# Optimization experiments

Hardware: AMD Instinct MI355X
Metric: run time of the kernel (lower is better)

## Reference

```python
import jax, jax.numpy as jnp
import numpy as np

W = 4  # kernel_size

def setup_inputs() -> dict:
    key = jax.random.key(0)
    k1, k2, k3, k4 = jax.random.split(key, 4)
    B, T, D, H = 4, 4096, 2048, 256
    x = jax.random.normal(k1, (B, T, D), dtype=jnp.float32)
    # stored as [in, out] (transpose of torch Linear convention)
    w1 = jax.random.normal(k2, (D, H), dtype=jnp.float32) * 0.02
    w2 = jax.random.normal(k3, (H, D * W), dtype=jnp.float32) * 0.02
    b2 = jax.random.normal(k4, (D * W,), dtype=jnp.float32) * 0.02
    return {"x": x, "w1": w1, "w2": w2, "b2": b2}

def reference(x, w1, w2, b2):
    # x: [B, T, D]
    B, T, D = x.shape
    # kernel generator: Linear -> silu -> Linear(+bias)
    h = jax.nn.silu(jnp.einsum('btd,dh->bth', x, w1))
    flat = jnp.einsum('bth,ho->bto', h, w2) + b2          # [B, T, D*W]
    kernels = flat.reshape(B, T, D, W)                    # per-token depthwise kernels
    # causal depthwise dynamic conv: out[t] = sum_w k[t, :, w] * x[t - (W-1) + w]
    xp = jnp.pad(x, ((0, 0), (W - 1, 0), (0, 0)))         # left-pad time by W-1
    out = jnp.zeros_like(x)
    for w in range(W):  # W is a small static constant (4)
        out = out + kernels[..., w] * xp[:, w:w + T, :]
    return jax.nn.silu(out)
```

## Files before the change

### kernel.cpp

```cpp
#include <hip/hip_runtime.h>

typedef unsigned short u16;
typedef unsigned int   u32;
typedef __attribute__((ext_vector_type(8))) short short8;
typedef __attribute__((ext_vector_type(4))) float floatx4;

#define T_DIM 4096
#define D_DIM 2048
#define H_DIM 256
#define M_DIM 16384
#define NFLAT 8192

__device__ __forceinline__ u16 f2bf(float f) {
  union { float f; u32 u; } c; c.f = f;
  u32 x = c.u;
  x += 0x7FFFu + ((x >> 16) & 1u);
  return (u16)(x >> 16);
}
__device__ __forceinline__ u32 pk2(float a, float b) {
  return (u32)f2bf(a) | ((u32)f2bf(b) << 16);
}

__device__ __forceinline__ void glds16(const void* g, void* l) {
  __builtin_amdgcn_global_load_lds(
      (const __attribute__((address_space(1))) void*)g,
      (__attribute__((address_space(3))) void*)l, 16, 0, 0);
}

__global__ void __launch_bounds__(256) tr_cvt_all(const float* __restrict__ w1,
                                                  u16* __restrict__ w1t,
                                                  const float* __restrict__ w2,
                                                  u16* __restrict__ w2t) {
  __shared__ u16 tile[32][33];
  int bid = blockIdx.x;
  const float* src; u16* dst; int R, C, c0, r0;
  if (bid < 512) {
    src = w1; dst = w1t; R = D_DIM; C = H_DIM;
    c0 = (bid & 7) * 32; r0 = (bid >> 3) * 32;
  } else {
    int b = bid - 512;
    src = w2; dst = w2t; R = H_DIM; C = NFLAT;
    c0 = (b & 255) * 32; r0 = (b >> 8) * 32;
  }
  const int tx = threadIdx.x & 31;
  const int ty = threadIdx.x >> 5;
  #pragma unroll
  for (int i = ty; i < 32; i += 8)
    tile[i][tx] = f2bf(src[(size_t)(r0 + i) * C + (c0 + tx)]);
  __syncthreads();
  #pragma unroll
  for (int i = ty; i < 32; i += 8)
    dst[(size_t)(c0 + i) * R + (r0 + tx)] = tile[tx][i];
}

__global__ void __launch_bounds__(256) gemm1_silu(const float* __restrict__ X,
                                                  const u16* __restrict__ Bt,
                                                  u16* __restrict__ H) {
  __shared__ __align__(16) u16 As[2][64][64];
  __shared__ __align__(16) u16 Bs[2][64][64];
  const int tid  = threadIdx.x;
  const int lane = tid & 63, l15 = lane & 15, quad = lane >> 4;
  const int wv   = tid >> 6, wy = wv >> 1, wx = wv & 1;
  const int lin  = blockIdx.x + blockIdx.y * 4;
  const int wgid = (lin & 7) * 128 + (lin >> 3);
  const int m0   = (wgid >> 2) * 64;
  const int n0   = (wgid & 3) * 64;
  const int srow = lane >> 3, sc = lane & 7;

  floatx4 acc[2][2];
  const floatx4 zf = {0.f, 0.f, 0.f, 0.f};
  #pragma unroll
  for (int i = 0; i < 2; ++i)
    #pragma unroll
    for (int j = 0; j < 2; ++j) acc[i][j] = zf;

  float4 fA[2][2];

#define G1_LOADA(KT)                                                          \
  _Pragma("unroll")                                                           \
  for (int i = 0; i < 2; ++i) {                                               \
    int s = i * 256 + tid, row = s >> 3, g = s & 7;                           \
    const float* xs = &X[(size_t)(m0 + row) * D_DIM + (KT) * 64 + g * 8];     \
    fA[i][0] = *(const float4*)xs;                                            \
    fA[i][1] = *(const float4*)(xs + 4);                                      \
  }

#define G1_WRITEA(BUF)                                                        \
  _Pragma("unroll")                                                           \
  for (int i = 0; i < 2; ++i) {                                               \
    int s = i * 256 + tid, row = s >> 3, g = s & 7, c = g ^ (row & 7);        \
    uint4 pk;                                                                 \
    pk.x = pk2(fA[i][0].x, fA[i][0].y);                                       \
    pk.y = pk2(fA[i][0].z, fA[i][0].w);                                       \
    pk.z = pk2(fA[i][1].x, fA[i][1].y);                                       \
    pk.w = pk2(fA[i][1].z, fA[i][1].w);                                       \
    *(uint4*)&As[BUF][row][c * 8] = pk;                                       \
  }

#define G1_STAGEB(KT, BUF)                                                    \
  _Pragma("unroll")                                                           \
  for (int ci = 0; ci < 2; ++ci) {                  \
    int ch  = wv * 2 + ci;                                                    \
    int row = ch * 8 + srow;                                                  \
    glds16(&Bt[(size_t)(n0 + row) * D_DIM + (KT) * 64 + (sc ^ (row & 7)) * 8],\
           (char*)Bs + (BUF) * 8192 + ch * 1024);                             \
  }

  G1_LOADA(0);
  G1_STAGEB(0, 0);
  G1_WRITEA(0);
  G1_LOADA(1);
  __syncthreads();

  #pragma unroll 2
  for (int t = 0; t < 32; ++t) {
    const int b = t & 1;
    if (t + 1 < 32) {
      G1_WRITEA(b ^ 1);
      G1_STAGEB(t + 1, b ^ 1);
    }
    if (t + 2 < 32) G1_LOADA(t + 2);
    short8 af[2][2], bfr[2][2];
    #pragma unroll
    for (int ks = 0; ks < 2; ++ks) {
      #pragma unroll
      for (int mi = 0; mi < 2; ++mi) {
        int row = wy * 32 + mi * 16 + l15;
        af[mi][ks] = *(const short8*)&As[b][row][((ks * 4 + quad) ^ (row & 7)) * 8];
      }
      #pragma unroll
      for (int ni = 0; ni < 2; ++ni) {
        int row = wx * 32 + ni * 16 + l15;
        bfr[ni][ks] = *(const short8*)&Bs[b][row][((ks * 4 + quad) ^ (row & 7)) * 8];
      }
    }
    #pragma unroll
    for (int ks = 0; ks < 2; ++ks)
      #pragma unroll
      for (int mi = 0; mi < 2; ++mi)
        #pragma unroll
        for (int ni = 0; ni < 2; ++ni)
          acc[mi][ni] = __builtin_amdgcn_mfma_f32_16x16x32_bf16(af[mi][ks], bfr[ni][ks], acc[mi][ni], 0, 0, 0);
    if (t + 1 < 32) __syncthreads();
  }

  #pragma unroll
  for (int mi = 0; mi < 2; ++mi)
    #pragma unroll
    for (int ni = 0; ni < 2; ++ni)
      #pragma unroll
      for (int r = 0; r < 4; ++r) {
        float v = acc[mi][ni][r];
        v = v / (1.f + __expf(-v));
        int row = m0 + wy * 32 + mi * 16 + quad * 4 + r;
        int col = n0 + wx * 32 + ni * 16 + l15;
        H[(size_t)row * H_DIM + col] = f2bf(v);
      }
#undef G1_LOADA
#undef G1_WRITEA
#undef G1_STAGEB
}

__global__ void __launch_bounds__(256) gemm2_conv_silu(const u16* __restrict__ Hin,
                                                       const u16* __restrict__ Bt,
                                                       const float* __restrict__ bias,
                                                       const float* __restrict__ X,
                                                       float* __restrict__ Out) {
  __shared__ __align__(16) u16 As[128][64];
  __shared__ __align__(16) u16 Bs[128][64];
  const int tid  = threadIdx.x;
  const int lane = tid & 63, l15 = lane & 15, quad = lane >> 4;
  const int wv   = tid >> 6, wy = wv >> 1, wx = wv & 1;
  const int lin  = blockIdx.x + blockIdx.y * 64;
  const int wgid = (lin & 7) * 1024 + (lin >> 3);
  const int m0   = (wgid >> 6) * 128;
  const int d0   = (wgid & 63) * 32;
  const int srow = lane >> 3, sc = lane & 7;

  floatx4 acc[4][4];
  const floatx4 zf = {0.f, 0.f, 0.f, 0.f};
  #pragma unroll
  for (int i = 0; i < 4; ++i)
    #pragma unroll
    for (int j = 0; j < 4; ++j) acc[i][j] = zf;

  for (int k0 = 0; k0 < H_DIM; k0 += 64) {
    __syncthreads();
    #pragma unroll
    for (int ci = 0; ci < 4; ++ci) {
      int ch  = ci * 4 + wv;
      int row = ch * 8 + srow;
      int g   = (sc ^ (row & 7)) * 8;
      glds16(&Hin[(size_t)(m0 + row) * H_DIM + k0 + g], (char*)As + ch * 1024);
      int fc = (d0 + ((row >> 6) << 4) + (row & 15)) * 4 + ((row >> 4) & 3);
      glds16(&Bt[(size_t)fc * H_DIM + k0 + g], (char*)Bs + ch * 1024);
    }
    __syncthreads();
    short8 af[4][2], bfr[4][2];
    #pragma unroll
    for (int ks = 0; ks < 2; ++ks) {
      #pragma unroll
      for (int mi = 0; mi < 4; ++mi) {
        int row = wy * 64 + mi * 16 + l15;
        af[mi][ks] = *(const short8*)&As[row][((ks * 4 + quad) ^ (row & 7)) * 8];
      }
      #pragma unroll
      for (int ni = 0; ni < 4; ++ni) {
        int row = wx * 64 + ni * 16 + l15;
        bfr[ni][ks] = *(const short8*)&Bs[row][((ks * 4 + quad) ^ (row & 7)) * 8];
      }
    }
    #pragma unroll
    for (int ks = 0; ks < 2; ++ks)
      #pragma unroll
      for (int mi = 0; mi < 4; ++mi)
        #pragma unroll
        for (int ni = 0; ni < 4; ++ni)
          acc[mi][ni] = __builtin_amdgcn_mfma_f32_16x16x32_bf16(af[mi][ks], bfr[ni][ks], acc[mi][ni], 0, 0, 0);
  }

  const int d     = d0 + wx * 16 + l15;
  const float4 bv = *(const float4*)&bias[(size_t)d * 4];
  const int tbase = m0 & (T_DIM - 1);
  const int bbase = m0 - tbase;
  const float* xcol = &X[(size_t)bbase * D_DIM + d];
  float* ocol       = &Out[(size_t)m0 * D_DIM + d];

  #pragma unroll
  for (int mi = 0; mi < 4; ++mi) {
    int t0 = wy * 64 + mi * 16 + quad * 4;
    int tq = tbase + t0;
    float xv[7];
    #pragma unroll
    for (int j = 0; j < 7; ++j) {
      int tt = tq - 3 + j;
      xv[j] = (tt >= 0) ? xcol[(size_t)tt * D_DIM] : 0.f;
    }
    #pragma unroll
    for (int r = 0; r < 4; ++r) {
      float c0 = acc[mi][0][r] + bv.x;
      float c1 = acc[mi][1][r] + bv.y;
      float c2 = acc[mi][2][r] + bv.z;
      float c3 = acc[mi][3][r] + bv.w;
      float o  = c0 * xv[r] + c1 * xv[r + 1] + c2 * xv[r + 2] + c3 * xv[r + 3];
      float y  = o / (1.f + __expf(-o));
      ocol[(size_t)(t0 + r) * D_DIM] = y;
    }
  }
}

extern "C" void kernel_launch(void* const* d_in, const int* in_sizes, int n_in,
                              void* d_out, int out_size, void* d_ws, size_t ws_size,
                              hipStream_t stream) {
  const float* x  = (const float*)d_in[0];
  const float* w1 = (const float*)d_in[1];
  const float* w2 = (const float*)d_in[2];
  const float* b2 = (const float*)d_in[3];
  float* out = (float*)d_out;

  u16* w1t = (u16*)d_ws;
  u16* w2t = w1t + (size_t)H_DIM * D_DIM;
  u16* h   = w2t + (size_t)NFLAT * H_DIM;

  tr_cvt_all<<<512 + 2048, 256, 0, stream>>>(w1, w1t, w2, w2t);
  gemm1_silu<<<dim3(4, M_DIM / 64), 256, 0, stream>>>(x, w1t, h);
  gemm2_conv_silu<<<dim3(D_DIM / 32, M_DIM / 128), 256, 0, stream>>>(h, w2t, b2, x, out);
}
```

Before: 380.8 us.

## Retile gemm1 to full-H 32-row tiles so X is read once

gemm1 now assigns each block 32 rows of X and all 256 H columns, with each wave owning 64 output columns. Before, four blocks per 64-row strip each re-read the same fp32 X rows, so X traffic drops roughly fourfold. The cost is a larger B tile staged in LDS per k-step (64KB double-buffered) and more accumulators per wave, which may lower occupancy. The XCD-aware block swizzles in both GEMMs are also removed in favour of plain block indexing.

```diff
diff --git a/kernel.cpp b/kernel.cpp
--- a/kernel.cpp
+++ b/kernel.cpp
@@ -56,54 +56,49 @@
 __global__ void __launch_bounds__(256) gemm1_silu(const float* __restrict__ X,
                                                   const u16* __restrict__ Bt,
                                                   u16* __restrict__ H) {
-  __shared__ __align__(16) u16 As[2][64][64];
-  __shared__ __align__(16) u16 Bs[2][64][64];
+  __shared__ __align__(16) u16 As[2][32][64];
+  __shared__ __align__(16) u16 Bs[2][256][64];
   const int tid  = threadIdx.x;
   const int lane = tid & 63, l15 = lane & 15, quad = lane >> 4;
-  const int wv   = tid >> 6, wy = wv >> 1, wx = wv & 1;
-  const int lin  = blockIdx.x + blockIdx.y * 4;
-  const int wgid = (lin & 7) * 128 + (lin >> 3);
-  const int m0   = (wgid >> 2) * 64;
-  const int n0   = (wgid & 3) * 64;
+  const int wv   = tid >> 6;
+  const int m0   = blockIdx.x * 32;
   const int srow = lane >> 3, sc = lane & 7;
 
-  floatx4 acc[2][2];
+  floatx4 acc[2][4];
   const floatx4 zf = {0.f, 0.f, 0.f, 0.f};
   #pragma unroll
   for (int i = 0; i < 2; ++i)
     #pragma unroll
-    for (int j = 0; j < 2; ++j) acc[i][j] = zf;
-
-  float4 fA[2][2];
+    for (int j = 0; j < 4; ++j) acc[i][j] = zf;
+
+  float4 fA[2];
 
 #define G1_LOADA(KT)                                                          \
-  _Pragma("unroll")                                                           \
-  for (int i = 0; i < 2; ++i) {                                               \
-    int s = i * 256 + tid, row = s >> 3, g = s & 7;                           \
+  {                                                                           \
+    int row = tid >> 3, g = tid & 7;                                          \
     const float* xs = &X[(size_t)(m0 + row) * D_DIM + (KT) * 64 + g * 8];     \
-    fA[i][0] = *(const float4*)xs;                                            \
-    fA[i][1] = *(const float4*)(xs + 4);                                      \
+    fA[0] = *(const float4*)xs;                                               \
+    fA[1] = *(const float4*)(xs + 4);                                         \
   }
 
 #define G1_WRITEA(BUF)                                                        \
-  _Pragma("unroll")                                                           \
-  for (int i = 0; i < 2; ++i) {                                               \
-    int s = i * 256 + tid, row = s >> 3, g = s & 7, c = g ^ (row & 7);        \
+  {                                                                           \
+    int row = tid >> 3, g = tid & 7, c = g ^ (row & 7);                       \
     uint4 pk;                                                                 \
-    pk.x = pk2(fA[i][0].x, fA[i][0].y);                                       \
-    pk.y = pk2(fA[i][0].z, fA[i][0].w);                                       \
-    pk.z = pk2(fA[i][1].x, fA[i][1].y);                                       \
-    pk.w = pk2(fA[i][1].z, fA[i][1].w);                                       \
+    pk.x = pk2(fA[0].x, fA[0].y);                                             \
+    pk.y = pk2(fA[0].z, fA[0].w);                                             \
+    pk.z = pk2(fA[1].x, fA[1].y);                                             \
+    pk.w = pk2(fA[1].z, fA[1].w);                                             \
     *(uint4*)&As[BUF][row][c * 8] = pk;                                       \
   }
 
 #define G1_STAGEB(KT, BUF)                                                    \
   _Pragma("unroll")                                                           \
-  for (int ci = 0; ci < 2; ++ci) {                  \
-    int ch  = wv * 2 + ci;                                                    \
-    int row = ch * 8 + srow;                                                  \
-    glds16(&Bt[(size_t)(n0 + row) * D_DIM + (KT) * 64 + (sc ^ (row & 7)) * 8],\
-           (char*)Bs + (BUF) * 8192 + ch * 1024);                             \
+  for (int ci = 0; ci < 8; ++ci) {                 \
+    int ch  = wv * 8 + ci;                                                    \
+    int row = ch * 8 + srow;                             \
+    glds16(&Bt[(size_t)row * D_DIM + (KT) * 64 + (sc ^ (row & 7)) * 8],       \
+           (char*)Bs + (BUF) * 32768 + ch * 1024);                            \
   }
 
   G1_LOADA(0);
@@ -120,17 +115,17 @@
       G1_STAGEB(t + 1, b ^ 1);
     }
     if (t + 2 < 32) G1_LOADA(t + 2);
-    short8 af[2][2], bfr[2][2];
+    short8 af[2][2], bfr[4][2];
     #pragma unroll
     for (int ks = 0; ks < 2; ++ks) {
       #pragma unroll
       for (int mi = 0; mi < 2; ++mi) {
-        int row = wy * 32 + mi * 16 + l15;
+        int row = mi * 16 + l15;
         af[mi][ks] = *(const short8*)&As[b][row][((ks * 4 + quad) ^ (row & 7)) * 8];
       }
       #pragma unroll
-      for (int ni = 0; ni < 2; ++ni) {
-        int row = wx * 32 + ni * 16 + l15;
+      for (int ni = 0; ni < 4; ++ni) {
+        int row = wv * 64 + ni * 16 + l15;
         bfr[ni][ks] = *(const short8*)&Bs[b][row][((ks * 4 + quad) ^ (row & 7)) * 8];
       }
     }
@@ -139,7 +134,7 @@
       #pragma unroll
       for (int mi = 0; mi < 2; ++mi)
         #pragma unroll
-        for (int ni = 0; ni < 2; ++ni)
+        for (int ni = 0; ni < 4; ++ni)
           acc[mi][ni] = __builtin_amdgcn_mfma_f32_16x16x32_bf16(af[mi][ks], bfr[ni][ks], acc[mi][ni], 0, 0, 0);
     if (t + 1 < 32) __syncthreads();
   }
@@ -147,13 +142,13 @@
   #pragma unroll
   for (int mi = 0; mi < 2; ++mi)
     #pragma unroll
-    for (int ni = 0; ni < 2; ++ni)
+    for (int ni = 0; ni < 4; ++ni)
       #pragma unroll
       for (int r = 0; r < 4; ++r) {
         float v = acc[mi][ni][r];
         v = v / (1.f + __expf(-v));
-        int row = m0 + wy * 32 + mi * 16 + quad * 4 + r;
-        int col = n0 + wx * 32 + ni * 16 + l15;
+        int row = m0 + mi * 16 + quad * 4 + r;
+        int col = wv * 64 + ni * 16 + l15;
         H[(size_t)row * H_DIM + col] = f2bf(v);
       }
 #undef G1_LOADA
@@ -171,10 +166,8 @@
   const int tid  = threadIdx.x;
   const int lane = tid & 63, l15 = lane & 15, quad = lane >> 4;
   const int wv   = tid >> 6, wy = wv >> 1, wx = wv & 1;
-  const int lin  = blockIdx.x + blockIdx.y * 64;
-  const int wgid = (lin & 7) * 1024 + (lin >> 3);
-  const int m0   = (wgid >> 6) * 128;
-  const int d0   = (wgid & 63) * 32;
+  const int m0   = blockIdx.y * 128;
+  const int d0   = blockIdx.x * 32;
   const int srow = lane >> 3, sc = lane & 7;
 
   floatx4 acc[4][4];
@@ -263,6 +256,6 @@
   u16* h   = w2t + (size_t)NFLAT * H_DIM;
 
   tr_cvt_all<<<512 + 2048, 256, 0, stream>>>(w1, w1t, w2, w2t);
-  gemm1_silu<<<dim3(4, M_DIM / 64), 256, 0, stream>>>(x, w1t, h);
+  gemm1_silu<<<M_DIM / 32, 256, 0, stream>>>(x, w1t, h);
   gemm2_conv_silu<<<dim3(D_DIM / 32, M_DIM / 128), 256, 0, stream>>>(h, w2t, b2, x, out);
 }
```

Measured after the change: 341.4 us. -10.3%, faster.
